# Kernel optimization log

Measured on AMD Instinct MI355X. Metric: run time of the kernel, lower is better.

The kernel has to match this reference:

```python
import jax, jax.numpy as jnp
import numpy as np
import math

D_MODEL = 128
N_HEADS = 8
D_K = D_MODEL // N_HEADS
D_FF = 512
N_LAYERS = 3
N_BUCKETS = 32
EPS = 1e-5
NEG_INF = -1e9
SCALE = 1.0 / math.sqrt(D_K)


def _hier_adj_np(N, L=8):
    # deterministic hierarchical edges from ExpanderGraphBuilder.build_hierarchical_edges
    stride = max(1, int(math.sqrt(N / L)))
    layer_size = N // L if L <= N else 1
    A = np.zeros((N, N), dtype=np.float32)
    for l in range(min(L, N)):
        start = l * layer_size
        end = min(start + layer_size, N)
        for i in range(start, end):
            A[i, max(start, i - stride):min(end, i + stride + 1)] = 1.0
            A[i, i] = 0.0
    return np.maximum(A, A.T)


def _build_mask(h, depot_idx=0):
    # h: (B,N,D). Returns additive mask (B,N+1,N+1) incl. global node.
    B, N, _ = h.shape
    k = min(max(1, math.ceil(math.log2(N))), N - 1)
    sq = jnp.sum(h * h, axis=-1)
    d2 = sq[:, :, None] + sq[:, None, :] - 2.0 * jnp.einsum('bnd,bmd->bnm', h, h)
    d2 = d2 + jnp.where(jnp.eye(N, dtype=bool), jnp.inf, 0.0)
    _, knn_idx = jax.lax.top_k(-d2, k)  # (B,N,k) nearest neighbors
    b_ix = jnp.arange(B)[:, None, None]
    i_ix = jnp.arange(N)[None, :, None]
    adj = jnp.zeros((B, N, N), dtype=h.dtype).at[b_ix, i_ix, knn_idx].set(1.0)
    adj = jnp.maximum(adj, adj.transpose(0, 2, 1))  # symmetrize knn
    adj = jnp.maximum(adj, jnp.asarray(_hier_adj_np(N))[None])
    adj = adj.at[:, depot_idx, :].set(1.0)
    adj = adj.at[:, :, depot_idx].set(1.0)
    adj = jnp.maximum(adj, jnp.eye(N, dtype=h.dtype)[None])
    full = jnp.ones((B, N + 1, N + 1), dtype=h.dtype).at[:, :N, :N].set(adj)
    return jnp.where(full > 0, 0.0, NEG_INF).astype(h.dtype)


def _inorm(x, w, b):
    # InstanceNorm1d over node dim per channel (x: (B,N1,D))
    mu = jnp.mean(x, axis=1, keepdims=True)
    var = jnp.mean(jnp.square(x - mu), axis=1, keepdims=True)
    return (x - mu) * jax.lax.rsqrt(var + EPS) * w + b


def _ega_layer(hg, bucket, mask, Wq, Wk, Wv, Wo, emb, W1, b1, W2, b2, n1w, n1b, n2w, n2b):
    B, N1, D = hg.shape
    heads = lambda x: x.reshape(B, N1, N_HEADS, D_K).transpose(0, 2, 1, 3)
    Q, K, V = heads(hg @ Wq.T), heads(hg @ Wk.T), heads(hg @ Wv.T)
    scores = jnp.einsum('bhnd,bhmd->bhnm', Q, K) * SCALE
    # rel_scores[b,h,i,j] = <Q[b,h,i], emb[bucket[b,i,j], h]> : contract with the
    # 32-entry table first, then gather - same math, no (B,H,N,N,Dk) intermediate.
    qe = jnp.einsum('bhnd,khd->bhnk', Q, emb.reshape(N_BUCKETS, N_HEADS, D_K))
    rel = jnp.take_along_axis(qe, jnp.broadcast_to(bucket[:, None], (B, N_HEADS, N1, N1)), axis=3)
    attn = jax.nn.softmax(scores + rel + mask[:, None], axis=-1)
    ctx = jnp.einsum('bhnm,bhmd->bhnd', attn, V).transpose(0, 2, 1, 3).reshape(B, N1, D)
    h1 = _inorm(hg + ctx @ Wo.T, n1w, n1b)
    ffn = jax.nn.relu(h1 @ W1.T + b1) @ W2.T + b2
    return _inorm(h1 + ffn, n2w, n2b)


def _forward(coords, in_W, in_b, gnode, Wq, Wk, Wv, Wo, emb, W1, b1, W2, b2,
             n1_w, n1_b, n2_w, n2_b, out_W, out_b):
    B, N, _ = coords.shape
    h = coords @ in_W.T + in_b
    g = jnp.broadcast_to(gnode, (B, 1, D_MODEL)).astype(h.dtype)
    # distance buckets over coords extended with the global node at (0,0)
    coords_ext = jnp.concatenate([coords, jnp.zeros((B, 1, 2), coords.dtype)], axis=1)
    diff = coords_ext[:, :, None, :] - coords_ext[:, None, :, :]
    dist = jax.lax.stop_gradient(jnp.sqrt(jnp.sum(diff * diff, axis=-1)))
    bucket = jnp.clip((dist * N_BUCKETS).astype(jnp.int32), 0, N_BUCKETS - 1)  # (B,N+1,N+1)
    pools = []
    for l in range(N_LAYERS):
        g = g + h.mean(axis=1, keepdims=True)
        hg = jnp.concatenate([h, g], axis=1)
        mask = _build_mask(jax.lax.stop_gradient(h))  # torch builds adj via .item(): detached
        hg = _ega_layer(hg, bucket, mask, Wq[l], Wk[l], Wv[l], Wo[l], emb[l],
                        W1[l], b1[l], W2[l], b2[l], n1_w[l], n1_b[l], n2_w[l], n2_b[l])
        h, g = hg[:, :N], hg[:, N:]
        pools.append(h.mean(axis=1))
    p_multi = jnp.stack(pools, axis=1).mean(axis=1)
    E_static = (h + p_multi[:, None, :]) @ out_W.T + out_b
    return E_static, p_multi


def setup_inputs():
    key = jax.random.key(0)
    ks = jax.random.split(key, 24)
    B, N, L = 2, 1024, N_LAYERS
    def nrm(k, shape, s=0.05):
        return jax.random.normal(k, shape, dtype=jnp.float32) * s
    return {
        'coords': jax.random.uniform(ks[0], (B, N, 2), dtype=jnp.float32),
        'in_W': nrm(ks[1], (D_MODEL, 2), 0.5),
        'in_b': nrm(ks[2], (D_MODEL,)),
        'gnode': nrm(ks[3], (1, 1, D_MODEL), 0.2),
        'Wq': nrm(ks[4], (L, D_MODEL, D_MODEL)),
        'Wk': nrm(ks[5], (L, D_MODEL, D_MODEL)),
        'Wv': nrm(ks[6], (L, D_MODEL, D_MODEL)),
        'Wo': nrm(ks[7], (L, D_MODEL, D_MODEL)),
        'emb': nrm(ks[8], (L, N_BUCKETS, N_HEADS * D_K)),
        'W1': nrm(ks[9], (L, D_FF, D_MODEL)),
        'b1': nrm(ks[10], (L, D_FF)),
        'W2': nrm(ks[11], (L, D_MODEL, D_FF)),
        'b2': nrm(ks[12], (L, D_MODEL)),
        'n1_w': jnp.ones((L, D_MODEL), jnp.float32) + nrm(ks[13], (L, D_MODEL)),
        'n1_b': nrm(ks[14], (L, D_MODEL)),
        'n2_w': jnp.ones((L, D_MODEL), jnp.float32) + nrm(ks[15], (L, D_MODEL)),
        'n2_b': nrm(ks[16], (L, D_MODEL)),
        'out_W': nrm(ks[17], (D_MODEL, D_MODEL)),
        'out_b': nrm(ks[18], (D_MODEL,)),
    }


def reference(coords, in_W, in_b, gnode, Wq, Wk, Wv, Wo, emb, W1, b1, W2, b2,
              n1_w, n1_b, n2_w, n2_b, out_W, out_b):
    return _forward(coords, in_W, in_b, gnode, Wq, Wk, Wv, Wo, emb, W1, b1, W2, b2,
                    n1_w, n1_b, n2_w, n2_b, out_W, out_b)
```

## Files before the change

### kernel.cpp

```cpp
#include <hip/hip_runtime.h>

#define BB 2
#define NN 1024
#define N1 1025
#define DM 128
#define NH 8
#define DK 16
#define DFF 512
#define NBUK 32
#define NLAYERS 3
#define KNN_K 10
#define ADJW 17
#define BSTR 1088
#define NSPLIT 8
#define BIGF 3.0e38f
#define SM_OFF 24.0f

#define PWQ_OFF 0
#define PWK_OFF 49152
#define PWV_OFF 98304
#define PWO_OFF 147456
#define PW1_OFF 196608
#define PW2_OFF 393216
#define PWOUT_OFF 589824
#define PWQE_OFF 606208
#define PW_TOT 704512

#define PBLK 344
#define NBNODE 1024
#define EBLK (NBNODE + BB)
#define BBLK 8713

#define KSEL_BLK 512
#define QKV_GX 33
#define QKV_BLK (QKV_GX * 40)
#define OSUM_N (BB * NH * N1 * 16)
#define LSUM_N (BB * NH * N1)
#define STAT_N (BB * DM)
#define ZTOT (OSUM_N + LSUM_N + 4 * STAT_N)

typedef __attribute__((ext_vector_type(8))) short bf8;
typedef __attribute__((ext_vector_type(4))) float f4;
typedef unsigned short u16;
typedef unsigned int u32;

__device__ __forceinline__ u16 f2bf(float x) {
  unsigned u = __float_as_uint(x);
  return (u16)((u + 0x7fff + ((u >> 16) & 1)) >> 16);
}
__device__ __forceinline__ float bf2f(u16 u) {
  return __uint_as_float(((unsigned)u) << 16);
}
__device__ __forceinline__ bf8 mk8(ushort4 a, ushort4 b) {
  bf8 r;
  r[0] = (short)a.x; r[1] = (short)a.y; r[2] = (short)a.z; r[3] = (short)a.w;
  r[4] = (short)b.x; r[5] = (short)b.y; r[6] = (short)b.z; r[7] = (short)b.w;
  return r;
}

__global__ __launch_bounds__(256) void init_kernel(
    const float* __restrict__ coords, const float* __restrict__ inW,
    const float* __restrict__ inb, const float* __restrict__ gnode,
    const float* __restrict__ Wq, const float* __restrict__ Wk,
    const float* __restrict__ Wv, const float* __restrict__ Wo,
    const float* __restrict__ W1, const float* __restrict__ W2,
    const float* __restrict__ oW, const float* __restrict__ emb,
    u16* __restrict__ PH, u16* __restrict__ PL,
    float* __restrict__ X, u16* __restrict__ XH, u16* __restrict__ XM,
    u16* __restrict__ XL, unsigned char* __restrict__ buckp) {
  int blk = blockIdx.x;
  if (blk < PBLK) {
    int idx = blk * 256 + threadIdx.x;
    if (idx >= 88064) return;
    if (idx >= 75776) {
      int rel = idx - 75776;
      int lane = rel & 63, g = rel >> 6;
      int ks = g & 3, nt = g >> 2;
      int n = nt * 16 + (lane & 15);
      int k = ks * 32 + (lane >> 4) * 8;
      int l = n >> 8; int c = n & 255; int h = c >> 5, bk = c & 31;
      const float* e = emb + ((size_t)l * NBUK + bk) * DM + h * DK;
      const float* wq = Wq + ((size_t)l * DM + h * DK) * DM;
      u16* ph = PH + (size_t)idx * 8;
      u16* pl = PL + (size_t)idx * 8;
      #pragma unroll
      for (int q = 0; q < 8; ++q) {
        float s = 0.f;
        #pragma unroll
        for (int d = 0; d < DK; ++d) s += e[d] * wq[(size_t)d * DM + k + q];
        u16 hh = f2bf(s);
        ph[q] = hh;
        pl[q] = f2bf(s - bf2f(hh));
      }
      return;
    }
    const float* W; int rel, Kdim;
    if (idx < 24576) {
      int seg = idx / 6144; rel = idx % 6144; Kdim = 128;
      W = seg == 0 ? Wq : seg == 1 ? Wk : seg == 2 ? Wv : Wo;
    } else if (idx < 49152) { rel = idx - 24576; Kdim = 128; W = W1; }
    else if (idx < 73728)   { rel = idx - 49152; Kdim = 512; W = W2; }
    else                    { rel = idx - 73728; Kdim = 128; W = oW; }
    int lane = rel & 63;
    int g = rel >> 6;
    int ksteps = Kdim >> 5;
    int ks = g % ksteps, nt = g / ksteps;
    int n = nt * 16 + (lane & 15);
    int k = ks * 32 + (lane >> 4) * 8;
    const float* p = W + (size_t)n * Kdim + k;
    u16* ph = PH + (size_t)idx * 8;
    u16* pl = PL + (size_t)idx * 8;
    #pragma unroll
    for (int q = 0; q < 8; ++q) {
      float x = p[q];
      u16 hh = f2bf(x);
      ph[q] = hh;
      pl[q] = f2bf(x - bf2f(hh));
    }
    return;
  }
  if (blk < PBLK + EBLK) {
    int eb = blk - PBLK;
    if (eb >= NBNODE) {
      int b = eb - NBNODE;
      int t = threadIdx.x;
      if (t >= 128) return;
      int lane = t & 63;
      float sx = 0.f, sy = 0.f;
      for (int n = lane; n < NN; n += 64) {
        float2 c = *(const float2*)(coords + (size_t)(b * NN + n) * 2);
        sx += c.x; sy += c.y;
      }
      #pragma unroll
      for (int o = 1; o < 64; o <<= 1) { sx += __shfl_xor(sx, o); sy += __shfl_xor(sy, o); }
      float mx = sx * (1.0f / NN), my = sy * (1.0f / NN);
      int d = t;
      size_t id = ((size_t)b * N1 + NN) * DM + d;
      float v = gnode[d] + inb[d] + mx * inW[d * 2 + 0] + my * inW[d * 2 + 1];
      X[id] = v;
      u16 hh = f2bf(v); float r1 = v - bf2f(hh);
      u16 mm = f2bf(r1);
      XH[id] = hh; XM[id] = mm; XL[id] = f2bf(r1 - bf2f(mm));
      return;
    }
    int idx = eb * 256 + threadIdx.x;
    if (idx >= BB * NN * DM) return;
    int d = idx % DM; int r = idx / DM; int n = r % NN; int b = r / NN;
    float cx = coords[(b * NN + n) * 2 + 0], cy = coords[(b * NN + n) * 2 + 1];
    size_t id = ((size_t)b * N1 + n) * DM + d;
    float v = cx * inW[d * 2 + 0] + cy * inW[d * 2 + 1] + inb[d];
    X[id] = v;
    u16 hh = f2bf(v); float r1 = v - bf2f(hh);
    u16 mm = f2bf(r1);
    XH[id] = hh; XM[id] = mm; XL[id] = f2bf(r1 - bf2f(mm));
    return;
  }
  int idx = (blk - PBLK - EBLK) * 256 + threadIdx.x;
  if (idx >= BB * N1 * BSTR) return;
  int j = idx % BSTR; int r = idx / BSTR; int i = r % N1; int b = r / N1;
  unsigned char v = 0;
  if (j < N1) {
    float xi = 0.f, yi = 0.f, xj = 0.f, yj = 0.f;
    if (i < NN) { xi = coords[(b * NN + i) * 2]; yi = coords[(b * NN + i) * 2 + 1]; }
    if (j < NN) { xj = coords[(b * NN + j) * 2]; yj = coords[(b * NN + j) * 2 + 1]; }
    float dx = xi - xj, dy = yi - yj;
    float dist = sqrtf(dx * dx + dy * dy);
    int bu = (int)(dist * 32.0f);
    bu = bu < 0 ? 0 : (bu > 31 ? 31 : bu);
    v = (unsigned char)bu;
  }
  buckp[idx] = v;
}

__global__ __launch_bounds__(256) void gram_kernel(
    const u16* __restrict__ XH, const u16* __restrict__ XM, const u16* __restrict__ XL,
    unsigned long long* __restrict__ adj, float* __restrict__ d2) {
  __shared__ __align__(16) u16 AsH[32][72];
  __shared__ __align__(16) u16 AsM[32][72];
  __shared__ __align__(16) u16 AsL[32][72];
  __shared__ __align__(16) u16 BsH[64][72];
  __shared__ __align__(16) u16 BsM[64][72];
  __shared__ __align__(16) u16 BsL[64][72];
  __shared__ float sqS[64];
  int b = blockIdx.z;
  int m0 = blockIdx.x * 32, n0 = blockIdx.y * 64;
  size_t boff = (size_t)b * N1;
  int t = threadIdx.x;

  {
    int flat = blockIdx.x + 32 * (blockIdx.y + 16 * blockIdx.z);
    int tid = flat * 256 + t;
    if (tid < BB * N1 * ADJW) adj[tid] = 0ull;
  }

  int lane = t & 63, w = t >> 6;
  int wm = (w >> 1) * 16, wn = (w & 1) * 32;
  int quad = lane >> 4, r16 = lane & 15;

  f4 acc0 = {0.f, 0.f, 0.f, 0.f}, acc1 = {0.f, 0.f, 0.f, 0.f};
  int ar = t >> 3, as_ = (t & 7) * 8;
  int br = t >> 2, bs_ = (t & 3) * 16;
  int sqrow = t >> 2, sqk = (t & 3) * 16;
  float mySq = 0.f;

  for (int k0 = 0; k0 < DM; k0 += 64) {
    {
      size_t src = (boff + m0 + ar) * DM + k0 + as_;
      *(bf8*)&AsH[ar][as_] = *(const bf8*)(XH + src);
      *(bf8*)&AsM[ar][as_] = *(const bf8*)(XM + src);
      *(bf8*)&AsL[ar][as_] = *(const bf8*)(XL + src);
    }
    {
      size_t src = (boff + n0 + br) * DM + k0 + bs_;
      *(bf8*)&BsH[br][bs_] = *(const bf8*)(XH + src);
      *(bf8*)&BsH[br][bs_ + 8] = *(const bf8*)(XH + src + 8);
      *(bf8*)&BsM[br][bs_] = *(const bf8*)(XM + src);
      *(bf8*)&BsM[br][bs_ + 8] = *(const bf8*)(XM + src + 8);
      *(bf8*)&BsL[br][bs_] = *(const bf8*)(XL + src);
      *(bf8*)&BsL[br][bs_ + 8] = *(const bf8*)(XL + src + 8);
    }
    __syncthreads();
    #pragma unroll
    for (int ks = 0; ks < 64; ks += 16) {
      int seg = (quad & 1) * 8;
      bf8 aHM = *(const bf8*)((quad < 2) ? &AsH[wm + r16][ks + seg] : &AsM[wm + r16][ks + seg]);
      bf8 aHL = *(const bf8*)((quad < 2) ? &AsH[wm + r16][ks + seg] : &AsL[wm + r16][ks + seg]);
      #pragma unroll
      for (int tt = 0; tt < 2; ++tt) {
        int nr = wn + tt * 16 + r16;
        bf8 bH = *(const bf8*)&BsH[nr][ks + seg];
        bf8 bM = *(const bf8*)&BsM[nr][ks + seg];
        bf8 b3 = *(const bf8*)((quad < 2) ? &BsL[nr][ks + seg] : &BsH[nr][ks + seg]);
        f4& a = tt ? acc1 : acc0;
        a = __builtin_amdgcn_mfma_f32_16x16x32_bf16(aHM, bH, a, 0, 0, 0);
        a = __builtin_amdgcn_mfma_f32_16x16x32_bf16(aHM, bM, a, 0, 0, 0);
        a = __builtin_amdgcn_mfma_f32_16x16x32_bf16(aHL, b3, a, 0, 0, 0);
      }
    }
    #pragma unroll
    for (int half = 0; half < 2; ++half) {
      bf8 hv = *(const bf8*)&BsH[sqrow][sqk + half * 8];
      bf8 mv = *(const bf8*)&BsM[sqrow][sqk + half * 8];
      bf8 lv = *(const bf8*)&BsL[sqrow][sqk + half * 8];
      #pragma unroll
      for (int q = 0; q < 8; ++q) {
        float x = (bf2f((u16)hv[q]) + bf2f((u16)mv[q])) + bf2f((u16)lv[q]);
        mySq += x * x;
      }
    }
    __syncthreads();
  }
  mySq += __shfl_xor(mySq, 1);
  mySq += __shfl_xor(mySq, 2);
  if ((t & 3) == 0) sqS[sqrow] = mySq;
  __syncthreads();

  #pragma unroll
  for (int tt = 0; tt < 2; ++tt) {
    f4 a = tt ? acc1 : acc0;
    int nl = wn + tt * 16 + r16;
    int n = n0 + nl;
    float sj = sqS[nl];
    #pragma unroll
    for (int reg = 0; reg < 4; ++reg) {
      int m = m0 + wm + quad * 4 + reg;
      float v = (m == n) ? BIGF : (sj - 2.f * a[reg]);
      d2[((size_t)b * NN + m) * NN + n] = v;
    }
  }
}

__global__ __launch_bounds__(256) void knnqkv_kernel(
    const float* __restrict__ d2, unsigned long long* __restrict__ adj,
    const u16* __restrict__ AH, const u16* __restrict__ AL,
    const u16* __restrict__ Pbase_H, const u16* __restrict__ Pbase_L,
    size_t offQ, size_t offK, size_t offV, size_t offE,
    u16* __restrict__ QH, u16* __restrict__ QL,
    u16* __restrict__ KH, u16* __restrict__ KL, u16* __restrict__ Vbf,
    float* __restrict__ qe_all, float* __restrict__ zbuf, int M) {
  __shared__ float dd[4][NN];
  {
    int ztid = blockIdx.x * 256 + threadIdx.x;
    if (ztid < ZTOT) zbuf[ztid] = 0.f;
  }
  int blk = blockIdx.x;
  if (blk < KSEL_BLK) {
    int b = blk / (NN / 4);
    int i0 = (blk % (NN / 4)) * 4;
    int t = threadIdx.x, lane = t & 63, w = t >> 6;

    const float4* src = (const float4*)(d2 + ((size_t)b * NN + i0) * NN);
    float4* dst = (float4*)&dd[0][0];
    #pragma unroll
    for (int x = 0; x < 4; ++x) dst[t + x * 256] = src[t + x * 256];
    __syncthreads();

    int i = i0 + w;
    for (int it = 0; it < KNN_K; ++it) {
      float bv = BIGF; int bi = 0x3fffffff;
      for (int j = lane; j < NN; j += 64) {
        float v = dd[w][j];
        if (v < bv) { bv = v; bi = j; }
      }
      #pragma unroll
      for (int o = 1; o < 64; o <<= 1) {
        float ov = __shfl_xor(bv, o); int oi = __shfl_xor(bi, o);
        if (ov < bv || (ov == bv && oi < bi)) { bv = ov; bi = oi; }
      }
      if (lane == 0) {
        dd[w][bi] = BIGF;
        atomicOr(&adj[((size_t)b * N1 + i) * ADJW + (bi >> 6)], 1ull << (bi & 63));
        atomicOr(&adj[((size_t)b * N1 + bi) * ADJW + (i >> 6)], 1ull << (i & 63));
      }
    }
    return;
  }
  int rel = blk - KSEL_BLK;
  int gx = rel % QKV_GX;
  int y = rel / QKV_GX;
  int z, nt;
  if (y < 8) { z = 0; nt = y; }
  else if (y < 16) { z = 1; nt = y - 8; }
  else if (y < 24) { z = 2; nt = y - 16; }
  else { z = 3; nt = y - 24; }
  size_t woff = z == 0 ? offQ : (z == 1 ? offK : (z == 2 ? offV : offE));
  const u16* PH = Pbase_H + woff;
  const u16* PL = Pbase_L + woff;
  int lane = threadIdx.x & 63;
  int quad = lane >> 4, r16 = lane & 15;
  int mt = gx * 4 + (threadIdx.x >> 6);
  f4 acc = {0.f, 0.f, 0.f, 0.f};
  int m0 = mt * 16;
  int mrow = m0 + r16; if (mrow >= M) mrow = M - 1;
  const u16* aph = AH + (size_t)mrow * DM + quad * 8;
  const u16* apl = AL + (size_t)mrow * DM + quad * 8;
  const u16* ph = PH + ((size_t)nt * 4 * 64 + lane) * 8;
  const u16* pl = PL + ((size_t)nt * 4 * 64 + lane) * 8;
  #pragma unroll
  for (int ks = 0; ks < 4; ++ks) {
    bf8 aH = *(const bf8*)(aph);
    bf8 aL = *(const bf8*)(apl);
    aph += 32; apl += 32;
    bf8 bH = *(const bf8*)(ph + (size_t)ks * 512);
    bf8 bL = *(const bf8*)(pl + (size_t)ks * 512);
    acc = __builtin_amdgcn_mfma_f32_16x16x32_bf16(aH, bH, acc, 0, 0, 0);
    acc = __builtin_amdgcn_mfma_f32_16x16x32_bf16(aH, bL, acc, 0, 0, 0);
    acc = __builtin_amdgcn_mfma_f32_16x16x32_bf16(aL, bH, acc, 0, 0, 0);
  }
  if (m0 >= M) return;
  int n = nt * 16 + r16;
  #pragma unroll
  for (int reg = 0; reg < 4; ++reg) {
    int m = m0 + quad * 4 + reg;
    if (m >= M) continue;
    float v = acc[reg];
    if (z == 3) {
      int b = m / N1, nr = m % N1;
      int h = n >> 5, bk = n & 31;
      qe_all[(((size_t)b * NH + h) * N1 + nr) * 32 + bk] = v;
      continue;
    }
    size_t oi = (size_t)m * DM + n;
    if (z == 0) {
      float sv = v * 0.25f;
      u16 hh = f2bf(sv);
      QH[oi] = hh;
      QL[oi] = f2bf(sv - bf2f(hh));
    } else if (z == 1) {
      u16 hh = f2bf(v);
      KH[oi] = hh;
      KL[oi] = f2bf(v - bf2f(hh));
    } else {
      Vbf[oi] = f2bf(v);
    }
  }
}

__global__ __launch_bounds__(256) void gemm_wo_kernel(
    const float* __restrict__ Osum, const float* __restrict__ lsum,
    const u16* __restrict__ PH, const u16* __restrict__ PL,
    const float* __restrict__ res, float* __restrict__ outF,
    float* __restrict__ sumY, float* __restrict__ sumY2, int M) {
  __shared__ float sA[2][16], sQ[2][16];
  int t = threadIdx.x;
  if (t < 32) {
    sA[t >> 4][t & 15] = 0.f;
    sQ[t >> 4][t & 15] = 0.f;
  }
  __syncthreads();
  int lane = t & 63;
  int quad = lane >> 4, r16 = lane & 15;
  int mt = blockIdx.x * 4 + (t >> 6), nt = blockIdx.y;
  f4 acc = {0.f, 0.f, 0.f, 0.f};
  int m0 = mt * 16;
  int mrow = m0 + r16; if (mrow >= M) mrow = M - 1;
  int b = mrow / N1, nr = mrow % N1;
  const u16* ph = PH + ((size_t)nt * 4 * 64 + lane) * 8;
  const u16* pl = PL + ((size_t)nt * 4 * 64 + lane) * 8;
  #pragma unroll
  for (int ks = 0; ks < 4; ++ks) {
    int k = ks * 32 + quad * 8;
    int h = k >> 4, d0 = k & 15;
    size_t base = (size_t)(b * NH + h) * N1 + nr;
    float inv = 1.0f / lsum[base];
    const float* op = Osum + base * 16 + d0;
    bf8 aH, aL;
    #pragma unroll
    for (int j = 0; j < 8; ++j) {
      float v = op[j] * inv;
      u16 hh = f2bf(v);
      aH[j] = (short)hh;
      aL[j] = (short)f2bf(v - bf2f(hh));
    }
    bf8 bH = *(const bf8*)(ph + (size_t)ks * 512);
    bf8 bL = *(const bf8*)(pl + (size_t)ks * 512);
    acc = __builtin_amdgcn_mfma_f32_16x16x32_bf16(aH, bH, acc, 0, 0, 0);
    acc = __builtin_amdgcn_mfma_f32_16x16x32_bf16(aH, bL, acc, 0, 0, 0);
    acc = __builtin_amdgcn_mfma_f32_16x16x32_bf16(aL, bH, acc, 0, 0, 0);
  }
  int n = nt * 16 + r16;
  if (m0 < M) {
    #pragma unroll
    for (int reg = 0; reg < 4; ++reg) {
      int m = m0 + quad * 4 + reg;
      if (m < M) {
        float v = acc[reg] + res[(size_t)m * DM + n];
        outF[(size_t)m * DM + n] = v;
        int mb2 = m / N1;
        atomicAdd(&sA[mb2][r16], v);
        atomicAdd(&sQ[mb2][r16], v * v);
      }
    }
  }
  __syncthreads();
  if (t < 32) {
    int bb = t >> 4, d = nt * 16 + (t & 15);
    atomicAdd(&sumY[bb * DM + d], sA[bb][t & 15]);
    atomicAdd(&sumY2[bb * DM + d], sQ[bb][t & 15]);
  }
}

__global__ __launch_bounds__(256) void gemm_w1_kernel(
    const float* __restrict__ Yb, const float* __restrict__ sumY,
    const float* __restrict__ sumY2, const float* __restrict__ n1w,
    const float* __restrict__ n1b,
    const u16* __restrict__ PH, const u16* __restrict__ PL,
    const float* __restrict__ bias,
    u16* __restrict__ outH, u16* __restrict__ outL, int M) {
  __shared__ float muS[STAT_N], scvS[STAT_N], shS[STAT_N];
  int t = threadIdx.x;
  {
    float mu = sumY[t] * (1.0f / N1);
    float var = sumY2[t] * (1.0f / N1) - mu * mu;
    int d = t & (DM - 1);
    muS[t] = mu;
    scvS[t] = rsqrtf(var + 1e-5f) * n1w[d];
    shS[t] = n1b[d];
  }
  __syncthreads();
  int lane = t & 63;
  int quad = lane >> 4, r16 = lane & 15;
  int mt = blockIdx.x * 4 + (t >> 6), nt = blockIdx.y;
  f4 acc = {0.f, 0.f, 0.f, 0.f};
  int m0 = mt * 16;
  int mrow = m0 + r16; if (mrow >= M) mrow = M - 1;
  int b = mrow / N1;
  const float* yp = Yb + (size_t)mrow * DM + quad * 8;
  const u16* ph = PH + ((size_t)nt * 4 * 64 + lane) * 8;
  const u16* pl = PL + ((size_t)nt * 4 * 64 + lane) * 8;
  #pragma unroll
  for (int ks = 0; ks < 4; ++ks) {
    int k = ks * 32 + quad * 8;
    bf8 aH, aL;
    #pragma unroll
    for (int half = 0; half < 2; ++half) {
      float4 yv = *(const float4*)(yp + ks * 32 + half * 4);
      float ya[4] = {yv.x, yv.y, yv.z, yv.w};
      #pragma unroll
      for (int q = 0; q < 4; ++q) {
        int sidx = b * DM + k + half * 4 + q;
        float nv = (ya[q] - muS[sidx]) * scvS[sidx] + shS[sidx];
        u16 hh = f2bf(nv);
        aH[half * 4 + q] = (short)hh;
        aL[half * 4 + q] = (short)f2bf(nv - bf2f(hh));
      }
    }
    bf8 bH = *(const bf8*)(ph + (size_t)ks * 512);
    bf8 bL = *(const bf8*)(pl + (size_t)ks * 512);
    acc = __builtin_amdgcn_mfma_f32_16x16x32_bf16(aH, bH, acc, 0, 0, 0);
    acc = __builtin_amdgcn_mfma_f32_16x16x32_bf16(aH, bL, acc, 0, 0, 0);
    acc = __builtin_amdgcn_mfma_f32_16x16x32_bf16(aL, bH, acc, 0, 0, 0);
  }
  if (m0 >= M) return;
  int n = nt * 16 + r16;
  #pragma unroll
  for (int reg = 0; reg < 4; ++reg) {
    int m = m0 + quad * 4 + reg;
    if (m < M) {
      float v = fmaxf(acc[reg] + bias[n], 0.f);
      size_t oi = (size_t)m * DFF + n;
      u16 hh = f2bf(v);
      outH[oi] = hh;
      outL[oi] = f2bf(v - bf2f(hh));
    }
  }
}

__global__ __launch_bounds__(256) void gemm_w2_kernel(
    const u16* __restrict__ AH, const u16* __restrict__ AL,
    const u16* __restrict__ PH, const u16* __restrict__ PL,
    const float* __restrict__ bias, const float* __restrict__ Yb,
    const float* __restrict__ sumY, const float* __restrict__ sumY2,
    const float* __restrict__ n1w, const float* __restrict__ n1b,
    float* __restrict__ outF, float* __restrict__ sumX, float* __restrict__ sumX2,
    float* __restrict__ gsave, int M) {
  __shared__ float muS[STAT_N], scvS[STAT_N], shS[STAT_N];
  __shared__ float sA[2][16], sQ[2][16];
  int t = threadIdx.x;
  {
    float mu = sumY[t] * (1.0f / N1);
    float var = sumY2[t] * (1.0f / N1) - mu * mu;
    int d = t & (DM - 1);
    muS[t] = mu;
    scvS[t] = rsqrtf(var + 1e-5f) * n1w[d];
    shS[t] = n1b[d];
  }
  if (t < 32) {
    sA[t >> 4][t & 15] = 0.f;
    sQ[t >> 4][t & 15] = 0.f;
  }
  __syncthreads();
  int lane = t & 63;
  int quad = lane >> 4, r16 = lane & 15;
  int mt = blockIdx.x * 4 + (t >> 6), nt = blockIdx.y;
  f4 acc = {0.f, 0.f, 0.f, 0.f};
  int m0 = mt * 16;
  int mrow = m0 + r16; if (mrow >= M) mrow = M - 1;
  const u16* aph = AH + (size_t)mrow * DFF + quad * 8;
  const u16* apl = AL + (size_t)mrow * DFF + quad * 8;
  const u16* ph = PH + ((size_t)nt * 16 * 64 + lane) * 8;
  const u16* pl = PL + ((size_t)nt * 16 * 64 + lane) * 8;
  #pragma unroll 4
  for (int ks = 0; ks < 16; ++ks) {
    bf8 aH = *(const bf8*)(aph);
    bf8 aL = *(const bf8*)(apl);
    aph += 32; apl += 32;
    bf8 bH = *(const bf8*)(ph + (size_t)ks * 512);
    bf8 bL = *(const bf8*)(pl + (size_t)ks * 512);
    acc = __builtin_amdgcn_mfma_f32_16x16x32_bf16(aH, bH, acc, 0, 0, 0);
    acc = __builtin_amdgcn_mfma_f32_16x16x32_bf16(aH, bL, acc, 0, 0, 0);
    acc = __builtin_amdgcn_mfma_f32_16x16x32_bf16(aL, bH, acc, 0, 0, 0);
  }
  int n = nt * 16 + r16;
  if (m0 < M) {
    #pragma unroll
    for (int reg = 0; reg < 4; ++reg) {
      int m = m0 + quad * 4 + reg;
      if (m < M) {
        int b = m / N1, mn2 = m % N1;
        int sidx = b * DM + n;
        float h1 = (Yb[(size_t)m * DM + n] - muS[sidx]) * scvS[sidx] + shS[sidx];
        float v = acc[reg] + bias[n] + h1;
        outF[(size_t)m * DM + n] = v;
        atomicAdd(&sA[b][r16], v);
        atomicAdd(&sQ[b][r16], v * v);
        if (mn2 == NN) gsave[sidx] = v;
      }
    }
  }
  __syncthreads();
  if (t < 32) {
    int bb = t >> 4, d = nt * 16 + (t & 15);
    atomicAdd(&sumX[bb * DM + d], sA[bb][t & 15]);
    atomicAdd(&sumX2[bb * DM + d], sQ[bb][t & 15]);
  }
}

__global__ __launch_bounds__(256) void xsplit2_kernel(
    float* __restrict__ X, const float* __restrict__ sumX, const float* __restrict__ sumX2,
    const float* __restrict__ gsave, const float* __restrict__ w, const float* __restrict__ b_,
    float* __restrict__ pool, u16* __restrict__ XH, u16* __restrict__ XM,
    u16* __restrict__ XL) {
  int idx = blockIdx.x * 256 + threadIdx.x;
  if (idx >= BB * N1 * DM) return;
  int d = idx % DM; int r = idx / DM; int n = r % N1; int b = r / N1;
  int sidx = b * DM + d;
  float sx = sumX[sidx];
  float mu = sx * (1.0f / N1);
  float var = sumX2[sidx] * (1.0f / N1) - mu * mu;
  float scv = rsqrtf(var + 1e-5f) * w[d];
  float sh = b_[d];
  float hmean = ((sx - gsave[sidx]) * (1.0f / NN) - mu) * scv + sh;
  float nv = (X[idx] - mu) * scv + sh;
  if (n == NN) nv += hmean;
  X[idx] = nv;
  u16 hh = f2bf(nv); float r1 = nv - bf2f(hh);
  u16 mm = f2bf(r1);
  XH[idx] = hh; XM[idx] = mm; XL[idx] = f2bf(r1 - bf2f(mm));
  if (n == 0) pool[sidx] = hmean;
}

#define CH 64
#define NCH 17
__global__ __launch_bounds__(128) void attn_kernel(
    const u16* __restrict__ QH, const u16* __restrict__ QL,
    const u16* __restrict__ KH, const u16* __restrict__ KL,
    const u16* __restrict__ Vbf, const float* __restrict__ qe_all,
    const unsigned char* __restrict__ buckp, const unsigned long long* __restrict__ adj,
    float* __restrict__ Osum, float* __restrict__ lsum) {
  __shared__ __align__(16) u16 KsHi[2][CH][20];
  __shared__ __align__(16) u16 KsLo[2][CH][20];
  __shared__ __align__(16) u16 Vt[2][DK][68];
  __shared__ __align__(16) u16 Ps[2][16][72];
  __shared__ __align__(16) float qe_s[2][16][36];
  __shared__ u32 maskS[32][6];
  __shared__ unsigned char buckS[2][32][68];

  int qt = blockIdx.x;
  int h = blockIdx.y & 7, b = blockIdx.y >> 3;
  int s = blockIdx.z;
  int c0 = (NCH * s) / NSPLIT, c1 = (NCH * (s + 1)) / NSPLIT;
  int nwm = 2 * (c1 - c0);
  int t = threadIdx.x, lane = t & 63, w = t >> 6;
  int quad = lane >> 4, r16 = lane & 15;
  int i0 = qt * 32;
  int iw = i0 + w * 16;
  int bh = b * NH + h;

  for (int x = t; x < 32 * nwm; x += 128) {
    int rr = x / nwm, ww = x % nwm;
    int gi = i0 + rr; if (gi > NN) gi = NN;
    int W = 2 * c0 + ww;
    u32 v;
    if (gi == 0 || gi == NN) {
      v = 0xffffffffu;
    } else {
      const u32* a32 = (const u32*)(adj + ((size_t)b * N1 + gi) * ADJW);
      v = a32[W];
      int bs = gi & ~127;
      int lo = gi - 11 < bs ? bs : gi - 11;
      int be = bs + 127;
      int hi = gi + 11 > be ? be : gi + 11;
      int aa = lo - 32 * W, bnd = hi - 32 * W;
      if (aa < 0) aa = 0; if (bnd > 31) bnd = 31;
      if (aa <= bnd) v |= (0xffffffffu << aa) & (0xffffffffu >> (31 - bnd));
      if (W == 0) v |= 1u;
      if (W == 32) v |= 1u;
      int dg = gi - 32 * W;
      if (dg >= 0 && dg < 32) v |= 1u << dg;
    }
    if (W == 32) v &= 1u;
    else if (W == 33) v = 0u;
    maskS[rr][ww] = v;
  }
  #pragma unroll
  for (int e = 0; e < 2; ++e) {
    int x = lane + e * 64;
    int rr = x >> 3, bk = (x & 7) * 4;
    int gi = iw + rr; if (gi > NN) gi = NN;
    f4 v = *(const f4*)(qe_all + (((size_t)b * NH + h) * N1 + gi) * 32 + bk);
    *(f4*)&qe_s[w][rr][bk] = v;
  }
  bf8 qfrag;
  {
    int gi = iw + r16; if (gi > NN) gi = NN;
    const u16* qsrc = (quad < 2 ? QH : QL) + ((size_t)(b * N1 + gi) * DM + h * DK + (quad & 1) * 8);
    qfrag = *(const bf8*)qsrc;
  }

  ushort4 khr[2], klr[2], vvr[2]; u32 bkr[4];
  auto load_chunk = [&](int c) {
    int j0 = c * CH;
    #pragma unroll
    for (int ii = 0; ii < 2; ++ii) {
      int x = t + ii * 128;
      int key = x >> 2, ds = (x & 3) * 4;
      int jg = j0 + key; if (jg > NN) jg = NN;
      size_t src = (size_t)(b * N1 + jg) * DM + h * DK + ds;
      khr[ii] = *(const ushort4*)(KH + src);
      klr[ii] = *(const ushort4*)(KL + src);
      vvr[ii] = *(const ushort4*)(Vbf + src);
    }
    #pragma unroll
    for (int ii = 0; ii < 4; ++ii) {
      int x = t + ii * 128;
      int rr = x >> 4, c4 = (x & 15) * 4;
      int gi = i0 + rr; if (gi > NN) gi = NN;
      bkr[ii] = *(const u32*)(buckp + ((size_t)b * N1 + gi) * BSTR + j0 + c4);
    }
  };
  auto store_chunk = [&](int pb) {
    #pragma unroll
    for (int ii = 0; ii < 2; ++ii) {
      int x = t + ii * 128;
      int key = x >> 2, ds = (x & 3) * 4;
      *(ushort4*)&KsHi[pb][key][ds] = khr[ii];
      *(ushort4*)&KsLo[pb][key][ds] = klr[ii];
      Vt[pb][ds + 0][key] = vvr[ii].x;
      Vt[pb][ds + 1][key] = vvr[ii].y;
      Vt[pb][ds + 2][key] = vvr[ii].z;
      Vt[pb][ds + 3][key] = vvr[ii].w;
    }
    #pragma unroll
    for (int ii = 0; ii < 4; ++ii) {
      int x = t + ii * 128;
      int rr = x >> 4, c4 = (x & 15) * 4;
      *(u32*)&buckS[pb][rr][c4] = bkr[ii];
    }
  };

  f4 Oacc = {0.f, 0.f, 0.f, 0.f};
  float lrun[4] = {0.f, 0.f, 0.f, 0.f};

  load_chunk(c0);
  store_chunk(0);

  for (int c = c0; c < c1; ++c) {
    int pb = (c - c0) & 1;
    bool pf = (c + 1 < c1);
    if (pf) load_chunk(c + 1);
    __syncthreads();

    f4 S[4];
    #pragma unroll
    for (int tt = 0; tt < 4; ++tt) {
      int key = tt * 16 + r16;
      int off = (quad & 1) * 8;
      bf8 bhv = mk8(*(const ushort4*)&KsHi[pb][key][off], *(const ushort4*)&KsHi[pb][key][off + 4]);
      bf8 blv = mk8(*(const ushort4*)&KsLo[pb][key][off], *(const ushort4*)&KsLo[pb][key][off + 4]);
      f4 z = {0.f, 0.f, 0.f, 0.f};
      z = __builtin_amdgcn_mfma_f32_16x16x32_bf16(qfrag, bhv, z, 0, 0, 0);
      z = __builtin_amdgcn_mfma_f32_16x16x32_bf16(qfrag, blv, z, 0, 0, 0);
      S[tt] = z;
    }

    #pragma unroll
    for (int rg = 0; rg < 4; ++rg) {
      int rowb = w * 16 + quad * 4 + rg;
      u32 mw0 = maskS[rowb][2 * (c - c0)];
      u32 mw1 = maskS[rowb][2 * (c - c0) + 1];
      float ps = 0.f;
      #pragma unroll
      for (int tt = 0; tt < 4; ++tt) {
        u32 mword = (tt & 2) ? mw1 : mw0;
        int bit = (tt & 1) * 16 + r16;
        int bk = buckS[pb][rowb][tt * 16 + r16] & 31;
        float rel = qe_s[w][quad * 4 + rg][bk];
        float sc = S[tt][rg] + rel;
        sc += ((mword >> bit) & 1u) ? 0.f : -1.0e9f;
        float p = __expf(sc - SM_OFF);
        ps += p;
        Ps[w][quad * 4 + rg][tt * 16 + r16] = f2bf(p);
      }
      #pragma unroll
      for (int o = 1; o < 16; o <<= 1) ps += __shfl_xor(ps, o);
      lrun[rg] += ps;
    }
    #pragma unroll
    for (int half = 0; half < 2; ++half) {
      bf8 pa = *(const bf8*)&Ps[w][r16][half * 32 + quad * 8];
      bf8 vb = mk8(*(const ushort4*)&Vt[pb][r16][half * 32 + quad * 8],
                   *(const ushort4*)&Vt[pb][r16][half * 32 + quad * 8 + 4]);
      Oacc = __builtin_amdgcn_mfma_f32_16x16x32_bf16(pa, vb, Oacc, 0, 0, 0);
    }

    if (pf) store_chunk(pb ^ 1);
  }

  #pragma unroll
  for (int rg = 0; rg < 4; ++rg) {
    int gi = i0 + w * 16 + quad * 4 + rg;
    if (gi < N1) {
      size_t base = (size_t)bh * N1 + gi;
      atomicAdd(&Osum[base * 16 + r16], Oacc[rg]);
      if (r16 == 0) atomicAdd(&lsum[base], lrun[rg]);
    }
  }
}

__global__ __launch_bounds__(256) void gemm_final_kernel(
    const float* __restrict__ X, const float* __restrict__ sumX,
    const float* __restrict__ sumX2, const float* __restrict__ gsave,
    const float* __restrict__ n2w, const float* __restrict__ n2b,
    const float* __restrict__ pools,
    const u16* __restrict__ PH, const u16* __restrict__ PL,
    const float* __restrict__ bias, float* __restrict__ out, float* __restrict__ out_pm) {
  __shared__ float muS[STAT_N], scvS[STAT_N], shS[STAT_N], pmS[STAT_N];
  int t = threadIdx.x;
  {
    float sx = sumX[t];
    float mu = sx * (1.0f / N1);
    float var = sumX2[t] * (1.0f / N1) - mu * mu;
    int d = t & (DM - 1);
    float scv = rsqrtf(var + 1e-5f) * n2w[d];
    float sh = n2b[d];
    float hmean = ((sx - gsave[t]) * (1.0f / NN) - mu) * scv + sh;
    float pm = (pools[t] + pools[BB * DM + t] + hmean) * (1.0f / 3.0f);
    muS[t] = mu; scvS[t] = scv; shS[t] = sh; pmS[t] = pm;
    if (blockIdx.x == 0 && blockIdx.y == 0) out_pm[t] = pm;
  }
  __syncthreads();
  int lane = t & 63;
  int quad = lane >> 4, r16 = lane & 15;
  int mt = blockIdx.x * 4 + (t >> 6), nt = blockIdx.y;
  const int M = BB * NN;
  f4 acc = {0.f, 0.f, 0.f, 0.f};
  int m0 = mt * 16;
  int mrow = m0 + r16; if (mrow >= M) mrow = M - 1;
  int mb = mrow / NN, mn = mrow % NN;
  const float* xp = X + ((size_t)mb * N1 + mn) * DM + quad * 8;
  const u16* ph = PH + ((size_t)nt * 4 * 64 + lane) * 8;
  const u16* pl = PL + ((size_t)nt * 4 * 64 + lane) * 8;
  #pragma unroll
  for (int ks = 0; ks < 4; ++ks) {
    int k = ks * 32 + quad * 8;
    bf8 aH, aL;
    #pragma unroll
    for (int half = 0; half < 2; ++half) {
      float4 xv = *(const float4*)(xp + ks * 32 + half * 4);
      float xa[4] = {xv.x, xv.y, xv.z, xv.w};
      #pragma unroll
      for (int q = 0; q < 4; ++q) {
        int sidx = mb * DM + k + half * 4 + q;
        float av = (xa[q] - muS[sidx]) * scvS[sidx] + shS[sidx] + pmS[sidx];
        u16 hh = f2bf(av);
        aH[half * 4 + q] = (short)hh;
        aL[half * 4 + q] = (short)f2bf(av - bf2f(hh));
      }
    }
    bf8 bH = *(const bf8*)(ph + (size_t)ks * 512);
    bf8 bL = *(const bf8*)(pl + (size_t)ks * 512);
    acc = __builtin_amdgcn_mfma_f32_16x16x32_bf16(aH, bH, acc, 0, 0, 0);
    acc = __builtin_amdgcn_mfma_f32_16x16x32_bf16(aH, bL, acc, 0, 0, 0);
    acc = __builtin_amdgcn_mfma_f32_16x16x32_bf16(aL, bH, acc, 0, 0, 0);
  }
  int n = nt * 16 + r16;
  #pragma unroll
  for (int reg = 0; reg < 4; ++reg) {
    int m = m0 + quad * 4 + reg;
    if (m < M) out[(size_t)m * DM + n] = acc[reg] + bias[n];
  }
}

extern "C" void kernel_launch(void* const* d_in, const int* in_sizes, int n_in,
                              void* d_out, int out_size, void* d_ws, size_t ws_size,
                              hipStream_t stream) {
  const float* coords = (const float*)d_in[0];
  const float* inW    = (const float*)d_in[1];
  const float* inb    = (const float*)d_in[2];
  const float* gnode  = (const float*)d_in[3];
  const float* Wq     = (const float*)d_in[4];
  const float* Wk     = (const float*)d_in[5];
  const float* Wv     = (const float*)d_in[6];
  const float* Wo     = (const float*)d_in[7];
  const float* emb    = (const float*)d_in[8];
  const float* W1     = (const float*)d_in[9];
  const float* b1     = (const float*)d_in[10];
  const float* W2     = (const float*)d_in[11];
  const float* b2     = (const float*)d_in[12];
  const float* n1w    = (const float*)d_in[13];
  const float* n1b    = (const float*)d_in[14];
  const float* n2w    = (const float*)d_in[15];
  const float* n2b    = (const float*)d_in[16];
  const float* outW   = (const float*)d_in[17];
  const float* outb   = (const float*)d_in[18];
  float* out = (float*)d_out;

  char* wsp = (char*)d_ws;
  size_t off = 0;
  auto alloc = [&](size_t bytes) -> void* {
    off = (off + 255) & ~(size_t)255;
    void* p = wsp + off;
    off += bytes;
    return p;
  };
  const size_t XB = (size_t)BB * N1 * DM * 4;
  const size_t HB = (size_t)BB * N1 * DM * 2;
  float* X0   = (float*)alloc(XB);
  float* X1   = (float*)alloc(XB);
  float* Yb   = (float*)alloc(XB);
  u16* XH = (u16*)alloc(HB); u16* XM = (u16*)alloc(HB); u16* XL = (u16*)alloc(HB);
  u16* QH = (u16*)alloc(HB); u16* QL = (u16*)alloc(HB);
  u16* KH = (u16*)alloc(HB); u16* KL = (u16*)alloc(HB);
  u16* Vbf = (u16*)alloc(HB);
  u16* FbH = (u16*)alloc((size_t)BB * N1 * DFF * 2);
  u16* FbL = (u16*)alloc((size_t)BB * N1 * DFF * 2);
  unsigned char* buckp = (unsigned char*)alloc((size_t)BB * N1 * BSTR);
  unsigned long long* adj = (unsigned long long*)alloc((size_t)BB * N1 * ADJW * 8);
  float* pools = (float*)alloc((size_t)NLAYERS * BB * DM * 4);
  float* qe_all = (float*)alloc((size_t)BB * NH * N1 * 32 * 4);
  float* zbuf = (float*)alloc((size_t)ZTOT * 4);
  float* gsave = (float*)alloc((size_t)STAT_N * 4);
  u16* PH = (u16*)alloc((size_t)PW_TOT * 2);
  u16* PL = (u16*)alloc((size_t)PW_TOT * 2);
  float* d2 = (float*)alloc((size_t)BB * NN * NN * 4);

  float* Osum = zbuf;
  float* lsum = zbuf + OSUM_N;
  float* sumY = zbuf + OSUM_N + LSUM_N;
  float* sumY2 = sumY + STAT_N;
  float* sumX = sumY2 + STAT_N;
  float* sumX2 = sumX + STAT_N;

  init_kernel<<<PBLK + EBLK + BBLK, 256, 0, stream>>>(
      coords, inW, inb, gnode, Wq, Wk, Wv, Wo, W1, W2, outW, emb,
      PH, PL, X0, XH, XM, XL, buckp);

  float* Xin = X0; float* Xout = X1;
  const int M = BB * N1;
  const int GX = 33;
  for (int l = 0; l < NLAYERS; ++l) {
    gram_kernel<<<dim3(32, 16, BB), 256, 0, stream>>>(XH, XM, XL, adj, d2);

    knnqkv_kernel<<<KSEL_BLK + QKV_BLK, 256, 0, stream>>>(
        d2, adj, XH, XM, PH, PL,
        (size_t)PWQ_OFF + (size_t)l * DM * DM,
        (size_t)PWK_OFF + (size_t)l * DM * DM,
        (size_t)PWV_OFF + (size_t)l * DM * DM,
        (size_t)PWQE_OFF + (size_t)l * 256 * DM,
        QH, QL, KH, KL, Vbf, qe_all, zbuf, M);

    attn_kernel<<<dim3(33, NH * BB, NSPLIT), 128, 0, stream>>>(
        QH, QL, KH, KL, Vbf, qe_all, buckp, adj, Osum, lsum);

    gemm_wo_kernel<<<dim3(GX, 8), 256, 0, stream>>>(
        Osum, lsum, PH + PWO_OFF + (size_t)l * DM * DM, PL + PWO_OFF + (size_t)l * DM * DM,
        Xin, Yb, sumY, sumY2, M);

    gemm_w1_kernel<<<dim3(GX, 32), 256, 0, stream>>>(
        Yb, sumY, sumY2, n1w + l * DM, n1b + l * DM,
        PH + PW1_OFF + (size_t)l * DFF * DM, PL + PW1_OFF + (size_t)l * DFF * DM,
        b1 + l * DFF, FbH, FbL, M);

    gemm_w2_kernel<<<dim3(GX, 8), 256, 0, stream>>>(
        FbH, FbL, PH + PW2_OFF + (size_t)l * DM * DFF, PL + PW2_OFF + (size_t)l * DM * DFF,
        b2 + l * DM, Yb, sumY, sumY2, n1w + l * DM, n1b + l * DM,
        Xout, sumX, sumX2, gsave, M);

    if (l < NLAYERS - 1) {
      xsplit2_kernel<<<(BB * N1 * DM + 255) / 256, 256, 0, stream>>>(
          Xout, sumX, sumX2, gsave, n2w + l * DM, n2b + l * DM,
          pools + (size_t)l * BB * DM, XH, XM, XL);
    }

    float* t2 = Xin; Xin = Xout; Xout = t2;
  }

  gemm_final_kernel<<<dim3(32, 8), 256, 0, stream>>>(
      Xin, sumX, sumX2, gsave, n2w + 2 * DM, n2b + 2 * DM, pools,
      PH + PWOUT_OFF, PL + PWOUT_OFF, outb, out, out + (size_t)BB * NN * DM);
}
```

Baseline: 382.3 us.

## Fuse Wo, W1, W2 and xsplit into one persistent kernel with grid barriers

After: 1.352 ms. 254% more time.

```diff
diff --git a/kernel.cpp b/kernel.cpp
--- a/kernel.cpp
+++ b/kernel.cpp
@@ -38,6 +38,10 @@
 #define LSUM_N (BB * NH * N1)
 #define STAT_N (BB * DM)
 #define ZTOT (OSUM_N + LSUM_N + 4 * STAT_N)
+#define ZBAR ZTOT
+#define ZTOT2 (ZTOT + 16)
+
+#define FFN_GRID 512
 
 typedef __attribute__((ext_vector_type(8))) short bf8;
 typedef __attribute__((ext_vector_type(4))) float f4;
@@ -56,6 +60,20 @@
   r[0] = (short)a.x; r[1] = (short)a.y; r[2] = (short)a.z; r[3] = (short)a.w;
   r[4] = (short)b.x; r[5] = (short)b.y; r[6] = (short)b.z; r[7] = (short)b.w;
   return r;
+}
+
+__device__ __forceinline__ void grid_sync(u32* bar, u32& target) {
+  __threadfence();
+  __syncthreads();
+  if (threadIdx.x == 0) {
+    target += FFN_GRID;
+    __hip_atomic_fetch_add(bar, 1u, __ATOMIC_RELEASE, __HIP_MEMORY_SCOPE_AGENT);
+    while (__hip_atomic_load(bar, __ATOMIC_ACQUIRE, __HIP_MEMORY_SCOPE_AGENT) < target) {
+      __builtin_amdgcn_s_sleep(2);
+    }
+  }
+  __syncthreads();
+  __threadfence();
 }
 
 __global__ __launch_bounds__(256) void init_kernel(
@@ -281,7 +299,7 @@
   __shared__ float dd[4][NN];
   {
     int ztid = blockIdx.x * 256 + threadIdx.x;
-    if (ztid < ZTOT) zbuf[ztid] = 0.f;
+    if (ztid < ZTOT2) zbuf[ztid] = 0.f;
   }
   int blk = blockIdx.x;
   if (blk < KSEL_BLK) {
@@ -376,13 +394,14 @@
   }
 }
 
-__global__ __launch_bounds__(256) void gemm_wo_kernel(
+__device__ void wo_body(int item,
     const float* __restrict__ Osum, const float* __restrict__ lsum,
     const u16* __restrict__ PH, const u16* __restrict__ PL,
     const float* __restrict__ res, float* __restrict__ outF,
     float* __restrict__ sumY, float* __restrict__ sumY2, int M) {
   __shared__ float sA[2][16], sQ[2][16];
   int t = threadIdx.x;
+  __syncthreads();
   if (t < 32) {
     sA[t >> 4][t & 15] = 0.f;
     sQ[t >> 4][t & 15] = 0.f;
@@ -390,7 +409,7 @@
   __syncthreads();
   int lane = t & 63;
   int quad = lane >> 4, r16 = lane & 15;
-  int mt = blockIdx.x * 4 + (t >> 6), nt = blockIdx.y;
+  int mt = (item % 33) * 4 + (t >> 6), nt = item / 33;
   f4 acc = {0.f, 0.f, 0.f, 0.f};
   int m0 = mt * 16;
   int mrow = m0 + r16; if (mrow >= M) mrow = M - 1;
@@ -440,7 +459,7 @@
   }
 }
 
-__global__ __launch_bounds__(256) void gemm_w1_kernel(
+__device__ void w1_body(int item,
     const float* __restrict__ Yb, const float* __restrict__ sumY,
     const float* __restrict__ sumY2, const float* __restrict__ n1w,
     const float* __restrict__ n1b,
@@ -449,6 +468,7 @@
     u16* __restrict__ outH, u16* __restrict__ outL, int M) {
   __shared__ float muS[STAT_N], scvS[STAT_N], shS[STAT_N];
   int t = threadIdx.x;
+  __syncthreads();
   {
     float mu = sumY[t] * (1.0f / N1);
     float var = sumY2[t] * (1.0f / N1) - mu * mu;
@@ -460,7 +480,7 @@
   __syncthreads();
   int lane = t & 63;
   int quad = lane >> 4, r16 = lane & 15;
-  int mt = blockIdx.x * 4 + (t >> 6), nt = blockIdx.y;
+  int mt = (item % 33) * 4 + (t >> 6), nt = item / 33;
   f4 acc = {0.f, 0.f, 0.f, 0.f};
   int m0 = mt * 16;
   int mrow = m0 + r16; if (mrow >= M) mrow = M - 1;
@@ -506,7 +526,7 @@
   }
 }
 
-__global__ __launch_bounds__(256) void gemm_w2_kernel(
+__device__ void w2_body(int item,
     const u16* __restrict__ AH, const u16* __restrict__ AL,
     const u16* __restrict__ PH, const u16* __restrict__ PL,
     const float* __restrict__ bias, const float* __restrict__ Yb,
@@ -517,6 +537,7 @@
   __shared__ float muS[STAT_N], scvS[STAT_N], shS[STAT_N];
   __shared__ float sA[2][16], sQ[2][16];
   int t = threadIdx.x;
+  __syncthreads();
   {
     float mu = sumY[t] * (1.0f / N1);
     float var = sumY2[t] * (1.0f / N1) - mu * mu;
@@ -532,7 +553,7 @@
   __syncthreads();
   int lane = t & 63;
   int quad = lane >> 4, r16 = lane & 15;
-  int mt = blockIdx.x * 4 + (t >> 6), nt = blockIdx.y;
+  int mt = (item % 33) * 4 + (t >> 6), nt = item / 33;
   f4 acc = {0.f, 0.f, 0.f, 0.f};
   int m0 = mt * 16;
   int mrow = m0 + r16; if (mrow >= M) mrow = M - 1;
@@ -576,12 +597,12 @@
   }
 }
 
-__global__ __launch_bounds__(256) void xsplit2_kernel(
+__device__ void xsplit2_body(int item,
     float* __restrict__ X, const float* __restrict__ sumX, const float* __restrict__ sumX2,
     const float* __restrict__ gsave, const float* __restrict__ w, const float* __restrict__ b_,
     float* __restrict__ pool, u16* __restrict__ XH, u16* __restrict__ XM,
     u16* __restrict__ XL) {
-  int idx = blockIdx.x * 256 + threadIdx.x;
+  int idx = item * 256 + threadIdx.x;
   if (idx >= BB * N1 * DM) return;
   int d = idx % DM; int r = idx / DM; int n = r % N1; int b = r / N1;
   int sidx = b * DM + d;
@@ -598,6 +619,37 @@
   u16 mm = f2bf(r1);
   XH[idx] = hh; XM[idx] = mm; XL[idx] = f2bf(r1 - bf2f(mm));
   if (n == 0) pool[sidx] = hmean;
+}
+
+__global__ __launch_bounds__(256, 2) void ffn_kernel(
+    const float* __restrict__ Osum, const float* __restrict__ lsum,
+    const u16* __restrict__ PH_wo, const u16* __restrict__ PL_wo,
+    const u16* __restrict__ PH_w1, const u16* __restrict__ PL_w1,
+    const u16* __restrict__ PH_w2, const u16* __restrict__ PL_w2,
+    const float* __restrict__ Xin, float* __restrict__ Yb,
+    const float* __restrict__ b1v, const float* __restrict__ b2v,
+    const float* __restrict__ n1w, const float* __restrict__ n1b,
+    const float* __restrict__ n2w, const float* __restrict__ n2b,
+    u16* __restrict__ FbH, u16* __restrict__ FbL,
+    float* __restrict__ Xout, float* __restrict__ sumY, float* __restrict__ sumY2,
+    float* __restrict__ sumX, float* __restrict__ sumX2, float* __restrict__ gsave,
+    float* __restrict__ pool, u16* __restrict__ XH, u16* __restrict__ XM,
+    u16* __restrict__ XL, u32* __restrict__ bar, int do_xsplit, int M) {
+  u32 target = 0;
+  for (int item = blockIdx.x; item < 264; item += FFN_GRID)
+    wo_body(item, Osum, lsum, PH_wo, PL_wo, Xin, Yb, sumY, sumY2, M);
+  grid_sync(bar, target);
+  for (int item = blockIdx.x; item < 1056; item += FFN_GRID)
+    w1_body(item, Yb, sumY, sumY2, n1w, n1b, PH_w1, PL_w1, b1v, FbH, FbL, M);
+  grid_sync(bar, target);
+  for (int item = blockIdx.x; item < 264; item += FFN_GRID)
+    w2_body(item, FbH, FbL, PH_w2, PL_w2, b2v, Yb, sumY, sumY2, n1w, n1b,
+            Xout, sumX, sumX2, gsave, M);
+  if (do_xsplit) {
+    grid_sync(bar, target);
+    for (int item = blockIdx.x; item < 1025; item += FFN_GRID)
+      xsplit2_body(item, Xout, sumX, sumX2, gsave, n2w, n2b, pool, XH, XM, XL);
+  }
 }
 
 #define CH 64
@@ -889,7 +941,7 @@
   unsigned long long* adj = (unsigned long long*)alloc((size_t)BB * N1 * ADJW * 8);
   float* pools = (float*)alloc((size_t)NLAYERS * BB * DM * 4);
   float* qe_all = (float*)alloc((size_t)BB * NH * N1 * 32 * 4);
-  float* zbuf = (float*)alloc((size_t)ZTOT * 4);
+  float* zbuf = (float*)alloc((size_t)ZTOT2 * 4);
   float* gsave = (float*)alloc((size_t)STAT_N * 4);
   u16* PH = (u16*)alloc((size_t)PW_TOT * 2);
   u16* PL = (u16*)alloc((size_t)PW_TOT * 2);
@@ -901,6 +953,7 @@
   float* sumY2 = sumY + STAT_N;
   float* sumX = sumY2 + STAT_N;
   float* sumX2 = sumX + STAT_N;
+  u32* bar = (u32*)(zbuf + ZBAR);
 
   init_kernel<<<PBLK + EBLK + BBLK, 256, 0, stream>>>(
       coords, inW, inb, gnode, Wq, Wk, Wv, Wo, W1, W2, outW, emb,
@@ -908,7 +961,6 @@
 
   float* Xin = X0; float* Xout = X1;
   const int M = BB * N1;
-  const int GX = 33;
   for (int l = 0; l < NLAYERS; ++l) {
     gram_kernel<<<dim3(32, 16, BB), 256, 0, stream>>>(XH, XM, XL, adj, d2);
 
@@ -923,25 +975,15 @@
     attn_kernel<<<dim3(33, NH * BB, NSPLIT), 128, 0, stream>>>(
         QH, QL, KH, KL, Vbf, qe_all, buckp, adj, Osum, lsum);
 
-    gemm_wo_kernel<<<dim3(GX, 8), 256, 0, stream>>>(
-        Osum, lsum, PH + PWO_OFF + (size_t)l * DM * DM, PL + PWO_OFF + (size_t)l * DM * DM,
-        Xin, Yb, sumY, sumY2, M);
-
-    gemm_w1_kernel<<<dim3(GX, 32), 256, 0, stream>>>(
-        Yb, sumY, sumY2, n1w + l * DM, n1b + l * DM,
+    ffn_kernel<<<FFN_GRID, 256, 0, stream>>>(
+        Osum, lsum,
+        PH + PWO_OFF + (size_t)l * DM * DM, PL + PWO_OFF + (size_t)l * DM * DM,
         PH + PW1_OFF + (size_t)l * DFF * DM, PL + PW1_OFF + (size_t)l * DFF * DM,
-        b1 + l * DFF, FbH, FbL, M);
-
-    gemm_w2_kernel<<<dim3(GX, 8), 256, 0, stream>>>(
-        FbH, FbL, PH + PW2_OFF + (size_t)l * DM * DFF, PL + PW2_OFF + (size_t)l * DM * DFF,
-        b2 + l * DM, Yb, sumY, sumY2, n1w + l * DM, n1b + l * DM,
-        Xout, sumX, sumX2, gsave, M);
-
-    if (l < NLAYERS - 1) {
-      xsplit2_kernel<<<(BB * N1 * DM + 255) / 256, 256, 0, stream>>>(
-          Xout, sumX, sumX2, gsave, n2w + l * DM, n2b + l * DM,
-          pools + (size_t)l * BB * DM, XH, XM, XL);
-    }
+        PH + PW2_OFF + (size_t)l * DM * DFF, PL + PW2_OFF + (size_t)l * DM * DFF,
+        Xin, Yb, b1 + l * DFF, b2 + l * DM,
+        n1w + l * DM, n1b + l * DM, n2w + l * DM, n2b + l * DM,
+        FbH, FbL, Xout, sumY, sumY2, sumX, sumX2, gsave,
+        pools + (size_t)l * BB * DM, XH, XM, XL, bar, (l < NLAYERS - 1) ? 1 : 0, M);
 
     float* t2 = Xin; Xin = Xout; Xout = t2;
   }
```
